# Kernel tuning notes

Hardware: AMD Instinct MI355X
Metric: run time of the kernel (lower is better)

## Reference

```python
import jax, jax.numpy as jnp
import numpy as np

EMBED_DIM = 1024
NUM_HEADS = 16
B, L = 4, 2048


def setup_inputs() -> dict:
    key = jax.random.key(0)
    ks = jax.random.split(key, 5)
    scale = 0.02
    return {
        "x": jax.random.normal(ks[0], (B, L, EMBED_DIM), dtype=jnp.float32),
        "Wqkv_w": jax.random.normal(ks[1], (3 * EMBED_DIM, EMBED_DIM), dtype=jnp.float32) * scale,
        "Wqkv_b": jax.random.normal(ks[2], (3 * EMBED_DIM,), dtype=jnp.float32) * scale,
        "out_w": jax.random.normal(ks[3], (EMBED_DIM, EMBED_DIM), dtype=jnp.float32) * scale,
        "out_b": jax.random.normal(ks[4], (EMBED_DIM,), dtype=jnp.float32) * scale,
    }


def reference(x, Wqkv_w, Wqkv_b, out_w, out_b):
    Bb, Ll, D = x.shape
    H = NUM_HEADS
    hd = D // H
    # fused QKV projection (torch Linear: x @ W.T + b)
    qkv = jnp.einsum("bld,ed->ble", x, Wqkv_w) + Wqkv_b  # [B, L, 3D]
    q, k, v = jnp.split(qkv, 3, axis=-1)
    # [B, H, L, hd]
    q = q.reshape(Bb, Ll, H, hd).transpose(0, 2, 1, 3)
    k = k.reshape(Bb, Ll, H, hd).transpose(0, 2, 1, 3)
    v = v.reshape(Bb, Ll, H, hd).transpose(0, 2, 1, 3)
    scale = 1.0 / jnp.sqrt(jnp.asarray(hd, dtype=x.dtype))
    scores = jnp.einsum("bhqd,bhkd->bhqk", q, k) * scale  # [B, H, L, L]
    # causal mask (upper triangle above diagonal masked)
    causal = jnp.tril(jnp.ones((Ll, Ll), dtype=bool))
    scores = jnp.where(causal, scores, jnp.asarray(-jnp.inf, dtype=scores.dtype))
    attn = jax.nn.softmax(scores, axis=-1)
    attn_out = jnp.einsum("bhqk,bhkd->bhqd", attn, v)  # [B, H, L, hd]
    attn_out = attn_out.transpose(0, 2, 1, 3).reshape(Bb, Ll, D)
    out = jnp.einsum("bld,ed->ble", attn_out, out_w) + out_b
    return out
```

## Files before the change

kernel.cpp:

```cpp
#include <hip/hip_runtime.h>
#include <stdint.h>

#define DEV __device__ __forceinline__

typedef unsigned short u16;
typedef __bf16 bf16x8 __attribute__((ext_vector_type(8)));
typedef float f32x4 __attribute__((ext_vector_type(4)));
typedef u16 u16x8 __attribute__((ext_vector_type(8)));

#define MFMA_BF16(A, B, C) __builtin_amdgcn_mfma_f32_16x16x32_bf16(A, B, C, 0, 0, 0)
#define EXP2(x) __builtin_amdgcn_exp2f(x)

DEV u16 f2bf(float f) {
    unsigned x;
    __builtin_memcpy(&x, &f, 4);
    unsigned r = (x + 0x7fffu + ((x >> 16) & 1u)) >> 16;
    return (u16)r;
}

DEV u16 f2bf_fast(float f) {
    unsigned x;
    __builtin_memcpy(&x, &f, 4);
    return (u16)((x + 0x8000u) >> 16);
}

DEV void storeC(u16* p, float v) { *p = f2bf(v); }
DEV void storeC(float* p, float v) { *p = v; }

DEV void async_copy16(const u16* g, u16* l) {
    __builtin_amdgcn_global_load_lds(
        (__attribute__((address_space(1))) unsigned int*)g,
        (__attribute__((address_space(3))) unsigned int*)l, 16, 0, 0);
}

constexpr int N_X = 8192 * 1024, N_WQ = 3072 * 1024, N_WO = 1024 * 1024;

__global__ __launch_bounds__(256)
void cvt_all(const float* __restrict__ x, const float* __restrict__ wq,
             const float* __restrict__ wo, u16* __restrict__ out) {
    const int i = (blockIdx.x * 256 + threadIdx.x) * 4;
    const float* src;
    if (i < N_X) src = x + i;
    else if (i < N_X + N_WQ) src = wq + (i - N_X);
    else src = wo + (i - N_X - N_WQ);
    const float4 v = *(const float4*)src;
    ushort4 o;
    o.x = f2bf(v.x);
    o.y = f2bf(v.y);
    o.z = f2bf(v.z);
    o.w = f2bf(v.w);
    *(ushort4*)(out + i) = o;
}

template <typename OT, bool VSPLIT>
__global__ __launch_bounds__(256, 2)
void gemm_bt_bias(const u16* __restrict__ A, const u16* __restrict__ Bw,
                  const float* __restrict__ bias, OT* __restrict__ C,
                  u16* __restrict__ vT, int M, int N, int K) {
    __shared__ __attribute__((aligned(16))) u16 sA[2][128 * 32];
    __shared__ __attribute__((aligned(16))) u16 sB[2][128 * 32];

    const int tid  = threadIdx.x;
    const int lane = tid & 63;
    const int wave = tid >> 6;
    const int m0 = blockIdx.x * 128;
    const int n0 = blockIdx.y * 128;
    const int wm = (wave & 1) * 64;
    const int wn = (wave >> 1) * 64;
    const int fr = lane & 15;
    const int q4 = lane >> 4;

    const int r0 = tid >> 2;
    const int c0 = (tid & 3) * 8;
    const u16* gA0 = A + (size_t)(m0 + r0) * K + c0;
    const u16* gA1 = A + (size_t)(m0 + 64 + r0) * K + c0;
    const u16* gB0 = Bw + (size_t)(n0 + r0) * K + c0;
    const u16* gB1 = Bw + (size_t)(n0 + 64 + r0) * K + c0;

    f32x4 acc[4][4];
#pragma unroll
    for (int i = 0; i < 4; i++)
#pragma unroll
        for (int j = 0; j < 4; j++) acc[i][j] = (f32x4){0.f, 0.f, 0.f, 0.f};

    for (int k0 = 0; k0 < K; k0 += 64) {
#pragma unroll
        for (int p = 0; p < 2; ++p) {
            async_copy16(gA0 + k0 + p * 32, &sA[p][tid * 8]);
            async_copy16(gA1 + k0 + p * 32, &sA[p][2048 + tid * 8]);
            async_copy16(gB0 + k0 + p * 32, &sB[p][tid * 8]);
            async_copy16(gB1 + k0 + p * 32, &sB[p][2048 + tid * 8]);
        }
        __syncthreads();

#pragma unroll
        for (int p = 0; p < 2; ++p) {
            bf16x8 af[4], bfr[4];
#pragma unroll
            for (int i = 0; i < 4; i++)
                af[i] = *(const bf16x8*)&sA[p][(wm + i * 16 + fr) * 32 + q4 * 8];
#pragma unroll
            for (int j = 0; j < 4; j++)
                bfr[j] = *(const bf16x8*)&sB[p][(wn + j * 16 + fr) * 32 + q4 * 8];
#pragma unroll
            for (int i = 0; i < 4; i++)
#pragma unroll
                for (int j = 0; j < 4; j++)
                    acc[i][j] = MFMA_BF16(af[i], bfr[j], acc[i][j]);
        }
        __syncthreads();
    }

#pragma unroll
    for (int j = 0; j < 4; j++) {
        const int col = n0 + wn + j * 16 + fr;
        const float bv = bias[col];
        if (VSPLIT && col >= 2048) {
#pragma unroll
            for (int i = 0; i < 4; i++) {
                const int row = m0 + wm + i * 16 + q4 * 4;
                ushort4 o;
                o.x = f2bf(acc[i][j][0] + bv);
                o.y = f2bf(acc[i][j][1] + bv);
                o.z = f2bf(acc[i][j][2] + bv);
                o.w = f2bf(acc[i][j][3] + bv);
                *(ushort4*)&vT[(size_t)(col - 2048) * 8192 + row] = o;
            }
        } else {
#pragma unroll
            for (int i = 0; i < 4; i++) {
                const int row = m0 + wm + i * 16 + q4 * 4;
#pragma unroll
                for (int r = 0; r < 4; r++)
                    storeC(&C[(size_t)(row + r) * N + col], acc[i][j][r] + bv);
            }
        }
    }
}

constexpr int Lc = 2048, Dc = 1024;

__global__ __launch_bounds__(256, 2)
void attn_fa(const u16* __restrict__ qkv, const u16* __restrict__ vT,
             u16* __restrict__ outb) {
    __shared__ __attribute__((aligned(16))) u16 sK[64 * 72];
    __shared__ __attribute__((aligned(16))) u16 sVT[64 * 72];
    __shared__ __attribute__((aligned(16))) u16 sP[4][4][16 * 72];

    const int tid  = threadIdx.x;
    const int lane = tid & 63;
    const int wave = tid >> 6;
    const int fr = lane & 15;
    const int q4 = lane >> 4;

    const int id = blockIdx.x;
    const int g  = (id & 7) + 8 * (id >> 6);
    const int bx = (id >> 3) & 7;
    const int h = g & 15;
    const int b = g >> 4;
    const int qA = bx, qB = 15 - bx, qC = 16 + bx, qD = 31 - bx;

    constexpr float CEXP = 0.18033688011112042f;

    bf16x8 qfA[2], qfB[2], qfC[2], qfD[2];
#define LOADQ(qf, qblk)                                                     \
    {                                                                       \
        const int qrow = (qblk) * 64 + wave * 16 + fr;                      \
        const u16* qp = qkv + ((size_t)(b * Lc + qrow) * 3) * Dc + h * 64;  \
        qf[0] = *(const bf16x8*)(qp + q4 * 8);                              \
        qf[1] = *(const bf16x8*)(qp + 32 + q4 * 8);                         \
    }
    LOADQ(qfA, qA) LOADQ(qfB, qB) LOADQ(qfC, qC) LOADQ(qfD, qD)
#undef LOADQ

    f32x4 oA[4], oB[4], oC[4], oD[4];
#pragma unroll
    for (int t = 0; t < 4; t++) {
        oA[t] = (f32x4){0.f, 0.f, 0.f, 0.f};
        oB[t] = (f32x4){0.f, 0.f, 0.f, 0.f};
        oC[t] = (f32x4){0.f, 0.f, 0.f, 0.f};
        oD[t] = (f32x4){0.f, 0.f, 0.f, 0.f};
    }
    float mA = -3.4e38f, lA = 0.f, mB = -3.4e38f, lB = 0.f;
    float mC = -3.4e38f, lC = 0.f, mD = -3.4e38f, lD = 0.f;

    const int q_local = wave * 16 + fr;

    const int rr = tid >> 3;
    const int oo = tid & 7;
    const u16* kg = qkv + ((size_t)(b * Lc) * 3 + 1) * Dc + h * 64 + oo * 8;
    const u16* vg = vT + (size_t)(h * 64) * 8192 + b * Lc + oo * 8;

    u16x8 kr[2], vr[2];
#pragma unroll
    for (int c = 0; c < 2; ++c) {
        kr[c] = *(const u16x8*)(kg + (size_t)(c * 32 + rr) * 3072);
        vr[c] = *(const u16x8*)(vg + (size_t)(c * 32 + rr) * 8192);
    }

    u16* sPA = &sP[wave][0][0];
    u16* sPB = &sP[wave][1][0];
    u16* sPC = &sP[wave][2][0];
    u16* sPD = &sP[wave][3][0];

#define SM_TILE(S, mS, lS, oS, sPp, qblk)                                   \
    {                                                                       \
        if (jb == (qblk)) {                                                 \
            _Pragma("unroll") for (int t = 0; t < 4; t++)                   \
                _Pragma("unroll") for (int r = 0; r < 4; r++)               \
                    if (t * 16 + q4 * 4 + r > q_local) S[t][r] = -1e30f;    \
        }                                                                   \
        float mx = S[0][0];                                                 \
        _Pragma("unroll") for (int t = 0; t < 4; t++)                       \
            _Pragma("unroll") for (int r = 0; r < 4; r++)                   \
                mx = fmaxf(mx, S[t][r]);                                    \
        mx = fmaxf(mx, __shfl_xor(mx, 16));                                 \
        mx = fmaxf(mx, __shfl_xor(mx, 32));                                 \
        const float mnew = fmaxf(mS, mx);                                   \
        const float alpha = EXP2((mS - mnew) * CEXP);                       \
        float sum = 0.f;                                                    \
        _Pragma("unroll") for (int t = 0; t < 4; t++) {                     \
            _Pragma("unroll") for (int r = 0; r < 4; r++) {                 \
                const float p = EXP2((S[t][r] - mnew) * CEXP);              \
                S[t][r] = p;                                                \
                sum += p;                                                   \
            }                                                               \
            ushort4 o;                                                      \
            o.x = f2bf_fast(S[t][0]);                                       \
            o.y = f2bf_fast(S[t][1]);                                       \
            o.z = f2bf_fast(S[t][2]);                                       \
            o.w = f2bf_fast(S[t][3]);                                       \
            *(ushort4*)&sPp[fr * 72 + t * 16 + q4 * 4] = o;                 \
        }                                                                   \
        sum += __shfl_xor(sum, 16);                                         \
        sum += __shfl_xor(sum, 32);                                         \
        lS = alpha * lS + sum;                                              \
        mS = mnew;                                                          \
        _Pragma("unroll") for (int t = 0; t < 4; t++)                       \
            _Pragma("unroll") for (int r = 0; r < 4; r++)                   \
                oS[t][r] *= alpha;                                          \
    }

    for (int jb = 0; jb <= qD; ++jb) {
        __syncthreads();
#pragma unroll
        for (int c = 0; c < 2; ++c) {
            *(u16x8*)&sK[(c * 32 + rr) * 72 + oo * 8] = kr[c];
            *(u16x8*)&sVT[(c * 32 + rr) * 72 + oo * 8] = vr[c];
        }
        __syncthreads();
        if (jb < qD) {
#pragma unroll
            for (int c = 0; c < 2; ++c) {
                kr[c] = *(const u16x8*)(kg + (size_t)((jb + 1) * 64 + c * 32 + rr) * 3072);
                vr[c] = *(const u16x8*)(vg + (size_t)(c * 32 + rr) * 8192 + (jb + 1) * 64);
            }
        }

        const bool doA = (jb <= qA);
        const bool doB = (jb <= qB);
        const bool doC = (jb <= qC);

        f32x4 sA_[4], sB_[4], sC_[4], sD_[4];
#pragma unroll
        for (int t = 0; t < 4; t++) {
            const bf16x8 kf0 = *(const bf16x8*)&sK[(t * 16 + fr) * 72 + q4 * 8];
            const bf16x8 kf1 = *(const bf16x8*)&sK[(t * 16 + fr) * 72 + 32 + q4 * 8];
            sD_[t] = (f32x4){0.f, 0.f, 0.f, 0.f};
            sD_[t] = MFMA_BF16(kf0, qfD[0], sD_[t]);
            sD_[t] = MFMA_BF16(kf1, qfD[1], sD_[t]);
            if (doC) {
                sC_[t] = (f32x4){0.f, 0.f, 0.f, 0.f};
                sC_[t] = MFMA_BF16(kf0, qfC[0], sC_[t]);
                sC_[t] = MFMA_BF16(kf1, qfC[1], sC_[t]);
            }
            if (doB) {
                sB_[t] = (f32x4){0.f, 0.f, 0.f, 0.f};
                sB_[t] = MFMA_BF16(kf0, qfB[0], sB_[t]);
                sB_[t] = MFMA_BF16(kf1, qfB[1], sB_[t]);
            }
            if (doA) {
                sA_[t] = (f32x4){0.f, 0.f, 0.f, 0.f};
                sA_[t] = MFMA_BF16(kf0, qfA[0], sA_[t]);
                sA_[t] = MFMA_BF16(kf1, qfA[1], sA_[t]);
            }
        }

        SM_TILE(sD_, mD, lD, oD, sPD, qD);
        if (doC) SM_TILE(sC_, mC, lC, oC, sPC, qC);
        if (doB) SM_TILE(sB_, mB, lB, oB, sPB, qB);
        if (doA) SM_TILE(sA_, mA, lA, oA, sPA, qA);

#pragma unroll
        for (int ks = 0; ks < 2; ++ks) {
            const bf16x8 pfD = *(const bf16x8*)&sPD[fr * 72 + ks * 32 + q4 * 8];
            bf16x8 pfC, pfB, pfA;
            if (doC) pfC = *(const bf16x8*)&sPC[fr * 72 + ks * 32 + q4 * 8];
            if (doB) pfB = *(const bf16x8*)&sPB[fr * 72 + ks * 32 + q4 * 8];
            if (doA) pfA = *(const bf16x8*)&sPA[fr * 72 + ks * 32 + q4 * 8];
#pragma unroll
            for (int t = 0; t < 4; t++) {
                const bf16x8 vf = *(const bf16x8*)&sVT[(t * 16 + fr) * 72 + ks * 32 + q4 * 8];
                oD[t] = MFMA_BF16(vf, pfD, oD[t]);
                if (doC) oC[t] = MFMA_BF16(vf, pfC, oC[t]);
                if (doB) oB[t] = MFMA_BF16(vf, pfB, oB[t]);
                if (doA) oA[t] = MFMA_BF16(vf, pfA, oA[t]);
            }
        }
    }
#undef SM_TILE

#define WR_OUT(oS, lS, qblk)                                                      \
    {                                                                             \
        const float rl = 1.0f / lS;                                               \
        u16* orow =                                                               \
            outb + (size_t)(b * Lc + (qblk) * 64 + wave * 16 + fr) * Dc + h * 64; \
        _Pragma("unroll") for (int t = 0; t < 4; t++) {                           \
            ushort4 o;                                                            \
            o.x = f2bf(oS[t][0] * rl);                                            \
            o.y = f2bf(oS[t][1] * rl);                                            \
            o.z = f2bf(oS[t][2] * rl);                                            \
            o.w = f2bf(oS[t][3] * rl);                                            \
            *(ushort4*)(orow + t * 16 + q4 * 4) = o;                              \
        }                                                                         \
    }
    WR_OUT(oA, lA, qA)
    WR_OUT(oB, lB, qB)
    WR_OUT(oC, lC, qC)
    WR_OUT(oD, lD, qD)
#undef WR_OUT
}

extern "C" void kernel_launch(void* const* d_in, const int* in_sizes, int n_in,
                              void* d_out, int out_size, void* d_ws, size_t ws_size,
                              hipStream_t stream) {
    const float* x    = (const float*)d_in[0];
    const float* wqkv = (const float*)d_in[1];
    const float* bqkv = (const float*)d_in[2];
    const float* wout = (const float*)d_in[3];
    const float* bout = (const float*)d_in[4];
    float* out = (float*)d_out;

    u16* qkv    = (u16*)d_ws;
    u16* attn   = qkv + (size_t)8192 * 3072;
    u16* xbf    = attn + (size_t)8192 * 1024;
    u16* wqkvbf = xbf + (size_t)8192 * 1024;
    u16* woutbf = wqkvbf + (size_t)3072 * 1024;
    u16* vT     = woutbf + (size_t)1024 * 1024;

    dim3 blk(256);
    cvt_all<<<(N_X + N_WQ + N_WO) / 1024, blk, 0, stream>>>(x, wqkv, wout, xbf);

    gemm_bt_bias<u16, true><<<dim3(8192 / 128, 3072 / 128), blk, 0, stream>>>(
        xbf, wqkvbf, bqkv, qkv, vT, 8192, 3072, 1024);
    attn_fa<<<dim3(512), blk, 0, stream>>>(qkv, vT, attn);
    gemm_bt_bias<float, false><<<dim3(8192 / 128, 1024 / 128), blk, 0, stream>>>(
        attn, woutbf, bout, out, nullptr, 8192, 1024, 1024);
}
```

Measured before the change: 270.7 us.

## Use two-wave 64x128 GEMM warp tiles and lazy softmax rescaling in attention

```diff
diff --git a/kernel.cpp b/kernel.cpp
--- a/kernel.cpp
+++ b/kernel.cpp
@@ -53,10 +53,10 @@
 }
 
 template <typename OT, bool VSPLIT>
-__global__ __launch_bounds__(256, 2)
-void gemm_bt_bias(const u16* __restrict__ A, const u16* __restrict__ Bw,
-                  const float* __restrict__ bias, OT* __restrict__ C,
-                  u16* __restrict__ vT, int M, int N, int K) {
+__global__ __launch_bounds__(128, 2)
+void gemm_bt2(const u16* __restrict__ A, const u16* __restrict__ Bw,
+              const float* __restrict__ bias, OT* __restrict__ C,
+              u16* __restrict__ vT, int M, int N, int K) {
     __shared__ __attribute__((aligned(16))) u16 sA[2][128 * 32];
     __shared__ __attribute__((aligned(16))) u16 sB[2][128 * 32];
 
@@ -65,55 +65,54 @@
     const int wave = tid >> 6;
     const int m0 = blockIdx.x * 128;
     const int n0 = blockIdx.y * 128;
-    const int wm = (wave & 1) * 64;
-    const int wn = (wave >> 1) * 64;
+    const int wm = wave * 64;
     const int fr = lane & 15;
     const int q4 = lane >> 4;
 
     const int r0 = tid >> 2;
     const int c0 = (tid & 3) * 8;
-    const u16* gA0 = A + (size_t)(m0 + r0) * K + c0;
-    const u16* gA1 = A + (size_t)(m0 + 64 + r0) * K + c0;
-    const u16* gB0 = Bw + (size_t)(n0 + r0) * K + c0;
-    const u16* gB1 = Bw + (size_t)(n0 + 64 + r0) * K + c0;
-
-    f32x4 acc[4][4];
+    const u16* gA = A + (size_t)(m0 + r0) * K + c0;
+    const u16* gB = Bw + (size_t)(n0 + r0) * K + c0;
+    const size_t r32 = (size_t)32 * K;
+
+    f32x4 acc[4][8];
 #pragma unroll
     for (int i = 0; i < 4; i++)
 #pragma unroll
-        for (int j = 0; j < 4; j++) acc[i][j] = (f32x4){0.f, 0.f, 0.f, 0.f};
+        for (int j = 0; j < 8; j++) acc[i][j] = (f32x4){0.f, 0.f, 0.f, 0.f};
 
     for (int k0 = 0; k0 < K; k0 += 64) {
 #pragma unroll
         for (int p = 0; p < 2; ++p) {
-            async_copy16(gA0 + k0 + p * 32, &sA[p][tid * 8]);
-            async_copy16(gA1 + k0 + p * 32, &sA[p][2048 + tid * 8]);
-            async_copy16(gB0 + k0 + p * 32, &sB[p][tid * 8]);
-            async_copy16(gB1 + k0 + p * 32, &sB[p][2048 + tid * 8]);
+#pragma unroll
+            for (int s = 0; s < 4; ++s) {
+                async_copy16(gA + s * r32 + k0 + p * 32, &sA[p][s * 1024 + tid * 8]);
+                async_copy16(gB + s * r32 + k0 + p * 32, &sB[p][s * 1024 + tid * 8]);
+            }
         }
         __syncthreads();
 
 #pragma unroll
         for (int p = 0; p < 2; ++p) {
-            bf16x8 af[4], bfr[4];
+            bf16x8 af[4], bfr[8];
 #pragma unroll
             for (int i = 0; i < 4; i++)
                 af[i] = *(const bf16x8*)&sA[p][(wm + i * 16 + fr) * 32 + q4 * 8];
 #pragma unroll
-            for (int j = 0; j < 4; j++)
-                bfr[j] = *(const bf16x8*)&sB[p][(wn + j * 16 + fr) * 32 + q4 * 8];
+            for (int j = 0; j < 8; j++)
+                bfr[j] = *(const bf16x8*)&sB[p][(j * 16 + fr) * 32 + q4 * 8];
 #pragma unroll
             for (int i = 0; i < 4; i++)
 #pragma unroll
-                for (int j = 0; j < 4; j++)
+                for (int j = 0; j < 8; j++)
                     acc[i][j] = MFMA_BF16(af[i], bfr[j], acc[i][j]);
         }
         __syncthreads();
     }
 
 #pragma unroll
-    for (int j = 0; j < 4; j++) {
-        const int col = n0 + wn + j * 16 + fr;
+    for (int j = 0; j < 8; j++) {
+        const int col = n0 + j * 16 + fr;
         const float bv = bias[col];
         if (VSPLIT && col >= 2048) {
 #pragma unroll
@@ -216,12 +215,19 @@
                 mx = fmaxf(mx, S[t][r]);                                    \
         mx = fmaxf(mx, __shfl_xor(mx, 16));                                 \
         mx = fmaxf(mx, __shfl_xor(mx, 32));                                 \
-        const float mnew = fmaxf(mS, mx);                                   \
-        const float alpha = EXP2((mS - mnew) * CEXP);                       \
+        if (!__all((mx - mS) <= 44.0f)) {                                   \
+            const float mnew = fmaxf(mS, mx);                               \
+            const float alpha = EXP2((mS - mnew) * CEXP);                   \
+            lS *= alpha;                                                    \
+            _Pragma("unroll") for (int t = 0; t < 4; t++)                   \
+                _Pragma("unroll") for (int r = 0; r < 4; r++)               \
+                    oS[t][r] *= alpha;                                      \
+            mS = mnew;                                                      \
+        }                                                                   \
         float sum = 0.f;                                                    \
         _Pragma("unroll") for (int t = 0; t < 4; t++) {                     \
             _Pragma("unroll") for (int r = 0; r < 4; r++) {                 \
-                const float p = EXP2((S[t][r] - mnew) * CEXP);              \
+                const float p = EXP2((S[t][r] - mS) * CEXP);                \
                 S[t][r] = p;                                                \
                 sum += p;                                                   \
             }                                                               \
@@ -234,11 +240,7 @@
         }                                                                   \
         sum += __shfl_xor(sum, 16);                                         \
         sum += __shfl_xor(sum, 32);                                         \
-        lS = alpha * lS + sum;                                              \
-        mS = mnew;                                                          \
-        _Pragma("unroll") for (int t = 0; t < 4; t++)                       \
-            _Pragma("unroll") for (int r = 0; r < 4; r++)                   \
-                oS[t][r] *= alpha;                                          \
+        lS += sum;                                                          \
     }
 
     for (int jb = 0; jb <= qD; ++jb) {
@@ -348,12 +350,11 @@
     u16* woutbf = wqkvbf + (size_t)3072 * 1024;
     u16* vT     = woutbf + (size_t)1024 * 1024;
 
-    dim3 blk(256);
-    cvt_all<<<(N_X + N_WQ + N_WO) / 1024, blk, 0, stream>>>(x, wqkv, wout, xbf);
-
-    gemm_bt_bias<u16, true><<<dim3(8192 / 128, 3072 / 128), blk, 0, stream>>>(
+    cvt_all<<<(N_X + N_WQ + N_WO) / 1024, dim3(256), 0, stream>>>(x, wqkv, wout, xbf);
+
+    gemm_bt2<u16, true><<<dim3(8192 / 128, 3072 / 128), dim3(128), 0, stream>>>(
         xbf, wqkvbf, bqkv, qkv, vT, 8192, 3072, 1024);
-    attn_fa<<<dim3(512), blk, 0, stream>>>(qkv, vT, attn);
-    gemm_bt_bias<float, false><<<dim3(8192 / 128, 1024 / 128), blk, 0, stream>>>(
+    attn_fa<<<dim3(512), dim3(256), 0, stream>>>(qkv, vT, attn);
+    gemm_bt2<float, false><<<dim3(8192 / 128, 1024 / 128), dim3(128), 0, stream>>>(
         attn, woutbf, bout, out, nullptr, 8192, 1024, 1024);
 }
```

New measurement: 270.3 us. No clear change (-0.1%).

## Double-buffer K/V tiles via async global-to-LDS copies with XOR swizzle and lazy rescale

Applied to the files above, without the earlier changes.

```diff
diff --git a/kernel.cpp b/kernel.cpp
--- a/kernel.cpp
+++ b/kernel.cpp
@@ -143,8 +143,8 @@
 __global__ __launch_bounds__(256, 2)
 void attn_fa(const u16* __restrict__ qkv, const u16* __restrict__ vT,
              u16* __restrict__ outb) {
-    __shared__ __attribute__((aligned(16))) u16 sK[64 * 72];
-    __shared__ __attribute__((aligned(16))) u16 sVT[64 * 72];
+    __shared__ __attribute__((aligned(16))) u16 sK[2][64 * 64];
+    __shared__ __attribute__((aligned(16))) u16 sVT[2][64 * 64];
     __shared__ __attribute__((aligned(16))) u16 sP[4][4][16 * 72];
 
     const int tid  = threadIdx.x;
@@ -152,6 +152,7 @@
     const int wave = tid >> 6;
     const int fr = lane & 15;
     const int q4 = lane >> 4;
+    const int f7 = fr & 7;
 
     const int id = blockIdx.x;
     const int g  = (id & 7) + 8 * (id >> 6);
@@ -186,16 +187,17 @@
 
     const int q_local = wave * 16 + fr;
 
-    const int rr = tid >> 3;
-    const int oo = tid & 7;
-    const u16* kg = qkv + ((size_t)(b * Lc) * 3 + 1) * Dc + h * 64 + oo * 8;
-    const u16* vg = vT + (size_t)(h * 64) * 8192 + b * Lc + oo * 8;
-
-    u16x8 kr[2], vr[2];
-#pragma unroll
-    for (int c = 0; c < 2; ++c) {
-        kr[c] = *(const u16x8*)(kg + (size_t)(c * 32 + rr) * 3072);
-        vr[c] = *(const u16x8*)(vg + (size_t)(c * 32 + rr) * 8192);
+    const int srow = tid >> 3;
+    const int schk = (tid & 7) ^ (srow & 7);
+    const u16* kg = qkv + ((size_t)(b * Lc + srow) * 3 + 1) * Dc + h * 64 + schk * 8;
+    const u16* vg = vT + (size_t)(h * 64 + srow) * 8192 + b * Lc + schk * 8;
+
+#define STAGE(bufi, jb1)                                                          \
+    _Pragma("unroll") for (int c = 0; c < 2; ++c) {                               \
+        async_copy16(kg + (size_t)((jb1) * 64 + c * 32) * 3072,                   \
+                     &sK[bufi][c * 2048 + tid * 8]);                              \
+        async_copy16(vg + (size_t)(c * 32) * 8192 + (jb1) * 64,                   \
+                     &sVT[bufi][c * 2048 + tid * 8]);                             \
     }
 
     u16* sPA = &sP[wave][0][0];
@@ -216,12 +218,19 @@
                 mx = fmaxf(mx, S[t][r]);                                    \
         mx = fmaxf(mx, __shfl_xor(mx, 16));                                 \
         mx = fmaxf(mx, __shfl_xor(mx, 32));                                 \
-        const float mnew = fmaxf(mS, mx);                                   \
-        const float alpha = EXP2((mS - mnew) * CEXP);                       \
+        if (!__all((mx - mS) <= 44.0f)) {                                   \
+            const float mnew = fmaxf(mS, mx);                               \
+            const float alpha = EXP2((mS - mnew) * CEXP);                   \
+            lS *= alpha;                                                    \
+            _Pragma("unroll") for (int t = 0; t < 4; t++)                   \
+                _Pragma("unroll") for (int r = 0; r < 4; r++)               \
+                    oS[t][r] *= alpha;                                      \
+            mS = mnew;                                                      \
+        }                                                                   \
         float sum = 0.f;                                                    \
         _Pragma("unroll") for (int t = 0; t < 4; t++) {                     \
             _Pragma("unroll") for (int r = 0; r < 4; r++) {                 \
-                const float p = EXP2((S[t][r] - mnew) * CEXP);              \
+                const float p = EXP2((S[t][r] - mS) * CEXP);                \
                 S[t][r] = p;                                                \
                 sum += p;                                                   \
             }                                                               \
@@ -234,28 +243,17 @@
         }                                                                   \
         sum += __shfl_xor(sum, 16);                                         \
         sum += __shfl_xor(sum, 32);                                         \
-        lS = alpha * lS + sum;                                              \
-        mS = mnew;                                                          \
-        _Pragma("unroll") for (int t = 0; t < 4; t++)                       \
-            _Pragma("unroll") for (int r = 0; r < 4; r++)                   \
-                oS[t][r] *= alpha;                                          \
-    }
+        lS += sum;                                                          \
+    }
+
+    STAGE(0, 0);
 
     for (int jb = 0; jb <= qD; ++jb) {
+        asm volatile("s_waitcnt vmcnt(0)" ::: "memory");
         __syncthreads();
-#pragma unroll
-        for (int c = 0; c < 2; ++c) {
-            *(u16x8*)&sK[(c * 32 + rr) * 72 + oo * 8] = kr[c];
-            *(u16x8*)&sVT[(c * 32 + rr) * 72 + oo * 8] = vr[c];
-        }
-        __syncthreads();
-        if (jb < qD) {
-#pragma unroll
-            for (int c = 0; c < 2; ++c) {
-                kr[c] = *(const u16x8*)(kg + (size_t)((jb + 1) * 64 + c * 32 + rr) * 3072);
-                vr[c] = *(const u16x8*)(vg + (size_t)(c * 32 + rr) * 8192 + (jb + 1) * 64);
-            }
-        }
+        if (jb < qD) STAGE((jb & 1) ^ 1, jb + 1);
+        const u16* cK = sK[jb & 1];
+        const u16* cV = sVT[jb & 1];
 
         const bool doA = (jb <= qA);
         const bool doB = (jb <= qB);
@@ -264,8 +262,9 @@
         f32x4 sA_[4], sB_[4], sC_[4], sD_[4];
 #pragma unroll
         for (int t = 0; t < 4; t++) {
-            const bf16x8 kf0 = *(const bf16x8*)&sK[(t * 16 + fr) * 72 + q4 * 8];
-            const bf16x8 kf1 = *(const bf16x8*)&sK[(t * 16 + fr) * 72 + 32 + q4 * 8];
+            const int row = (t * 16 + fr) * 64;
+            const bf16x8 kf0 = *(const bf16x8*)&cK[row + (q4 ^ f7) * 8];
+            const bf16x8 kf1 = *(const bf16x8*)&cK[row + ((4 + q4) ^ f7) * 8];
             sD_[t] = (f32x4){0.f, 0.f, 0.f, 0.f};
             sD_[t] = MFMA_BF16(kf0, qfD[0], sD_[t]);
             sD_[t] = MFMA_BF16(kf1, qfD[1], sD_[t]);
@@ -300,7 +299,8 @@
             if (doA) pfA = *(const bf16x8*)&sPA[fr * 72 + ks * 32 + q4 * 8];
 #pragma unroll
             for (int t = 0; t < 4; t++) {
-                const bf16x8 vf = *(const bf16x8*)&sVT[(t * 16 + fr) * 72 + ks * 32 + q4 * 8];
+                const bf16x8 vf =
+                    *(const bf16x8*)&cV[(t * 16 + fr) * 64 + ((ks * 4 + q4) ^ f7) * 8];
                 oD[t] = MFMA_BF16(vf, pfD, oD[t]);
                 if (doC) oC[t] = MFMA_BF16(vf, pfC, oC[t]);
                 if (doB) oB[t] = MFMA_BF16(vf, pfB, oB[t]);
@@ -309,6 +309,7 @@
         }
     }
 #undef SM_TILE
+#undef STAGE
 
 #define WR_OUT(oS, lS, qblk)                                                      \
     {                                                                             \
```

New measurement: 268.8 us. About the same (-0.7%).
